# Kernel tuning notes

Measured on AMD Instinct MI355X. Metric: run time of the kernel, lower is better.

The kernel has to match this reference:

```python
import jax, jax.numpy as jnp
import numpy as np

HIDDEN = 2048
N_HEADS = 16
N_KV_HEADS = 8
HEAD_DIM = 128
ROTARY_DIM = 32  # int(128 * 0.25), already even
ROPE_THETA = 10000000.0
EPS = 1e-6
BATCH, SEQ = 2, 2048


def _rmsnorm(x, w, eps=EPS):
    # per-head RMSNorm over last dim; weight is zero-init, scale = 1 + w
    r = jax.lax.rsqrt(jnp.mean(x * x, axis=-1, keepdims=True) + eps)
    return x * r * (1.0 + w)


def _rope(x, positions, rotary_dim, theta):
    # x: [b, s, h, rotary_dim]; rotate-halves RoPE
    half = rotary_dim // 2
    inv_freq = 1.0 / (theta ** (jnp.arange(half, dtype=jnp.float32) / half))
    ang = positions.astype(jnp.float32)[:, :, None] * inv_freq  # [b, s, half]
    cos = jnp.cos(ang)[:, :, None, :]
    sin = jnp.sin(ang)[:, :, None, :]
    x1, x2 = x[..., :half], x[..., half:]
    return jnp.concatenate([x1 * cos - x2 * sin, x1 * sin + x2 * cos], axis=-1)


def setup_inputs() -> dict:
    key = jax.random.key(0)
    ks = jax.random.split(key, 8)
    scale = lambda fan_in: 1.0 / np.sqrt(fan_in)
    x = jax.random.normal(ks[0], (BATCH, SEQ, HIDDEN), dtype=jnp.float32)
    Wq = jax.random.normal(ks[1], (HIDDEN, N_HEADS * HEAD_DIM * 2), jnp.float32) * scale(HIDDEN)
    Wk = jax.random.normal(ks[2], (HIDDEN, N_KV_HEADS * HEAD_DIM), jnp.float32) * scale(HIDDEN)
    Wv = jax.random.normal(ks[3], (HIDDEN, N_KV_HEADS * HEAD_DIM), jnp.float32) * scale(HIDDEN)
    Wo = jax.random.normal(ks[4], (N_HEADS * HEAD_DIM, HIDDEN), jnp.float32) * scale(N_HEADS * HEAD_DIM)
    q_norm_w = jax.random.normal(ks[5], (HEAD_DIM,), jnp.float32) * 0.02
    k_norm_w = jax.random.normal(ks[6], (HEAD_DIM,), jnp.float32) * 0.02
    attention_mask = jnp.ones((BATCH, SEQ), dtype=jnp.int32)
    positions = jnp.broadcast_to(jnp.arange(SEQ, dtype=jnp.int32), (BATCH, SEQ))
    return {"x": x, "attention_mask": attention_mask, "positions": positions,
            "Wq": Wq, "Wk": Wk, "Wv": Wv, "Wo": Wo,
            "q_norm_w": q_norm_w, "k_norm_w": k_norm_w}


def reference(x, attention_mask, positions, Wq, Wk, Wv, Wo, q_norm_w, k_norm_w):
    b, s, _ = x.shape
    g = N_HEADS // N_KV_HEADS  # GQA group size

    q_all = jnp.einsum('bsh,ho->bso', x, Wq).reshape(b, s, N_HEADS, HEAD_DIM * 2)
    q, gate = jnp.split(q_all, 2, axis=-1)          # each [b,s,H,D]
    gate = gate.reshape(b, s, N_HEADS * HEAD_DIM)
    q = _rmsnorm(q, q_norm_w)
    k = _rmsnorm(jnp.einsum('bsh,ho->bso', x, Wk).reshape(b, s, N_KV_HEADS, HEAD_DIM), k_norm_w)
    v = jnp.einsum('bsh,ho->bso', x, Wv).reshape(b, s, N_KV_HEADS, HEAD_DIM)

    # partial RoPE on first ROTARY_DIM dims
    q = jnp.concatenate([_rope(q[..., :ROTARY_DIM], positions, ROTARY_DIM, ROPE_THETA), q[..., ROTARY_DIM:]], axis=-1)
    k = jnp.concatenate([_rope(k[..., :ROTARY_DIM], positions, ROTARY_DIM, ROPE_THETA), k[..., ROTARY_DIM:]], axis=-1)

    # grouped-query causal attention
    qg = q.reshape(b, s, N_KV_HEADS, g, HEAD_DIM)
    scores = jnp.einsum('bqhgd,bkhd->bhgqk', qg, k) / jnp.sqrt(jnp.float32(HEAD_DIM))
    causal = jnp.tril(jnp.ones((s, s), dtype=bool))
    key_valid = attention_mask.astype(bool)[:, None, None, None, :]  # [b,1,1,1,k]
    mask = causal[None, None, None, :, :] & key_valid
    scores = jnp.where(mask, scores, jnp.finfo(scores.dtype).min)
    probs = jax.nn.softmax(scores, axis=-1)
    attn = jnp.einsum('bhgqk,bkhd->bqhgd', probs, v).reshape(b, s, N_HEADS * HEAD_DIM)

    attn = attn * jax.nn.sigmoid(gate)
    return jnp.einsum('bso,oh->bsh', attn, Wo)
```

## Files before the change

### kernel.cpp

```cpp
#include <hip/hip_runtime.h>
#include <cstdint>

typedef __bf16  bf16;
typedef __bf16  bf16x8 __attribute__((ext_vector_type(8)));
typedef __bf16  bf16x4 __attribute__((ext_vector_type(4)));
typedef __bf16  bf16x2 __attribute__((ext_vector_type(2)));
typedef float   f32x4  __attribute__((ext_vector_type(4)));
typedef float   f32x16 __attribute__((ext_vector_type(16)));

#define GLOAD_LDS16(g, l) __builtin_amdgcn_global_load_lds( \
    (const __attribute__((address_space(1))) void*)(g),     \
    (__attribute__((address_space(3))) void*)(l), 16, 0, 0)

#define SEQ   2048
#define HID   2048
#define NH    16
#define NKV   8
#define HD    128
#define NQKV  6144
#define MTOT  4096

__device__ __forceinline__ void transw_body(const float* __restrict__ W, bf16* __restrict__ WT,
                                            int N, int n0, int k0, int t) {
    __shared__ float tile[64][65];
    int tn = t & 63, t4 = t >> 6;
    #pragma unroll
    for (int i = 0; i < 16; ++i) {
        int kk = i * 4 + t4;
        tile[kk][tn] = W[(size_t)(k0 + kk) * N + n0 + tn];
    }
    __syncthreads();
    int tk8 = (t & 7) * 8;
    int tnn = t >> 3;
    #pragma unroll
    for (int i = 0; i < 2; ++i) {
        int nn = i * 32 + tnn;
        bf16x8 o;
        #pragma unroll
        for (int j = 0; j < 8; ++j) o[j] = (bf16)tile[tk8 + j][nn];
        *(bf16x8*)(&WT[(size_t)(n0 + nn) * HID + k0 + tk8]) = o;
    }
}

__global__ __launch_bounds__(256) void prep_kernel(const float* __restrict__ x, bf16* __restrict__ xb,
                                                   const float* __restrict__ Wq, const float* __restrict__ Wk,
                                                   const float* __restrict__ Wv, const float* __restrict__ Wo,
                                                   bf16* __restrict__ wqkvT, bf16* __restrict__ woT) {
    int bx = blockIdx.x, t = threadIdx.x;
    if (bx < 4096) {
        int i = bx * 256 + t;
        f32x4 v0 = ((const f32x4*)x)[i * 2];
        f32x4 v1 = ((const f32x4*)x)[i * 2 + 1];
        bf16x8 o;
        o[0] = (bf16)v0[0]; o[1] = (bf16)v0[1]; o[2] = (bf16)v0[2]; o[3] = (bf16)v0[3];
        o[4] = (bf16)v1[0]; o[5] = (bf16)v1[1]; o[6] = (bf16)v1[2]; o[7] = (bf16)v1[3];
        ((bf16x8*)xb)[i] = o;
    } else if (bx < 4096 + 2048) {
        int idx = bx - 4096;
        transw_body(Wq, wqkvT, 4096, (idx & 63) * 64, (idx >> 6) * 64, t);
    } else if (bx < 4096 + 2048 + 512) {
        int idx = bx - (4096 + 2048);
        transw_body(Wk, wqkvT + (size_t)4096 * HID, 1024, (idx & 15) * 64, (idx >> 4) * 64, t);
    } else if (bx < 4096 + 2048 + 1024) {
        int idx = bx - (4096 + 2048 + 512);
        transw_body(Wv, wqkvT + (size_t)5120 * HID, 1024, (idx & 15) * 64, (idx >> 4) * 64, t);
    } else {
        int idx = bx - (4096 + 2048 + 1024);
        transw_body(Wo, woT, 2048, (idx & 31) * 64, (idx >> 5) * 64, t);
    }
}

template<bool OUT_BF16>
__global__ __launch_bounds__(256) void gemm_bt(const bf16* __restrict__ A, const bf16* __restrict__ Bt,
                                               void* __restrict__ C, int M, int N, int K) {
    __shared__ __align__(16) bf16 As[128 * 64];
    __shared__ __align__(16) bf16 Bs[128 * 64];
    const int tid = threadIdx.x;
    const int wave = tid >> 6, lane = tid & 63;
    const int l31 = lane & 31, half = lane >> 5;
    const int tile_n = blockIdx.x * 128, tile_m = blockIdx.y * 128;
    const int wm = (wave & 1) * 64, wn = (wave >> 1) * 64;
    const int sw = l31 & 7;
    f32x16 acc[2][2] = {};

    for (int k0 = 0; k0 < K; k0 += 64) {
        __syncthreads();
        #pragma unroll
        for (int j = 0; j < 4; ++j) {
            int s = j * 256 + tid;
            int row = s >> 3, c = s & 7;
            int cs = c ^ (row & 7);
            GLOAD_LDS16(A  + (size_t)(tile_m + row) * K + k0 + (cs << 3), As + (size_t)s * 8);
            GLOAD_LDS16(Bt + (size_t)(tile_n + row) * K + k0 + (cs << 3), Bs + (size_t)s * 8);
        }
        __syncthreads();
        #pragma unroll
        for (int ks = 0; ks < 4; ++ks) {
            int ch = ((ks * 2 + half) ^ sw) << 3;
            bf16x8 a0 = *(const bf16x8*)(As + (size_t)(wm + l31) * 64 + ch);
            bf16x8 a1 = *(const bf16x8*)(As + (size_t)(wm + 32 + l31) * 64 + ch);
            bf16x8 b0 = *(const bf16x8*)(Bs + (size_t)(wn + l31) * 64 + ch);
            bf16x8 b1 = *(const bf16x8*)(Bs + (size_t)(wn + 32 + l31) * 64 + ch);
            acc[0][0] = __builtin_amdgcn_mfma_f32_32x32x16_bf16(a0, b0, acc[0][0], 0, 0, 0);
            acc[0][1] = __builtin_amdgcn_mfma_f32_32x32x16_bf16(a0, b1, acc[0][1], 0, 0, 0);
            acc[1][0] = __builtin_amdgcn_mfma_f32_32x32x16_bf16(a1, b0, acc[1][0], 0, 0, 0);
            acc[1][1] = __builtin_amdgcn_mfma_f32_32x32x16_bf16(a1, b1, acc[1][1], 0, 0, 0);
        }
    }
    #pragma unroll
    for (int mt = 0; mt < 2; ++mt)
        #pragma unroll
        for (int nt = 0; nt < 2; ++nt)
            #pragma unroll
            for (int reg = 0; reg < 16; ++reg) {
                int row = tile_m + wm + mt * 32 + (reg & 3) + ((reg >> 2) * 8) + half * 4;
                int col = tile_n + wn + nt * 32 + l31;
                float v = acc[mt][nt][reg];
                if (OUT_BF16) ((bf16*)C)[(size_t)row * N + col] = (bf16)v;
                else          ((float*)C)[(size_t)row * N + col] = v;
            }
}

__global__ __launch_bounds__(256) void post_kernel(const bf16* __restrict__ qkv,
                                                   const float* __restrict__ qnw, const float* __restrict__ knw,
                                                   const int* __restrict__ positions,
                                                   bf16* __restrict__ Qh, bf16* __restrict__ Kh,
                                                   bf16* __restrict__ VT) {
    int bx = blockIdx.x;
    if (bx < 4096) {
        int tk = bx;
        int b = tk >> 11, s = tk & 2047;
        int wave = threadIdx.x >> 6, lane = threadIdx.x & 63;
        int g16 = lane >> 4;
        int l16 = lane & 15;
        int d0 = l16 * 8;
        float pos = (float)positions[tk];
        const float L = 1.4533435415278355f;

        float cv[8], sv[8];
        if (l16 < 4) {
            #pragma unroll
            for (int j = 0; j < 8; ++j) {
                float a = pos * exp2f(-(float)((l16 & 1) * 8 + j) * L);
                cv[j] = cosf(a); sv[j] = sinf(a);
            }
        }

        #pragma unroll
        for (int i = 0; i < 2; ++i) {
            int slot = i * 16 + wave * 4 + g16;
            if (slot >= 24) continue;
            bool isq = (slot < 16);
            int h = isq ? slot : slot - 16;
            const bf16* base = qkv + (size_t)tk * NQKV + (isq ? h * 256 : 4096 + h * HD) + d0;
            bf16x8 v = *(const bf16x8*)base;
            float f[8];
            float ssq = 0.0f;
            #pragma unroll
            for (int j = 0; j < 8; ++j) { f[j] = (float)v[j]; ssq += f[j] * f[j]; }
            #pragma unroll
            for (int off = 8; off; off >>= 1) ssq += __shfl_xor(ssq, off);
            float rn = rsqrtf(ssq * (1.0f / 128.0f) + 1e-6f);
            const float* nw = isq ? qnw : knw;
            f32x4 wa = *(const f32x4*)(nw + d0);
            f32x4 wb = *(const f32x4*)(nw + d0 + 4);
            float xv[8];
            #pragma unroll
            for (int j = 0; j < 4; ++j) { xv[j] = f[j] * rn * (1.0f + wa[j]); xv[j + 4] = f[j + 4] * rn * (1.0f + wb[j]); }
            float out[8];
            #pragma unroll
            for (int j = 0; j < 8; ++j) out[j] = xv[j];
            if (l16 < 4) {
                #pragma unroll
                for (int j = 0; j < 8; ++j) {
                    float p = __shfl_xor(xv[j], 2);
                    out[j] = (l16 < 2) ? (xv[j] * cv[j] - p * sv[j])
                                       : (xv[j] * cv[j] + p * sv[j]);
                }
            }
            bf16x8 o;
            #pragma unroll
            for (int j = 0; j < 8; ++j) o[j] = (bf16)out[j];
            bf16* dst = isq ? (Qh + ((size_t)(b * NH + h) * SEQ + s) * HD)
                            : (Kh + ((size_t)(b * NKV + h) * SEQ + s) * HD);
            *(bf16x8*)(dst + d0) = o;
        }
    } else {
        int idx = bx - 4096;
        int bh = idx >> 5, st = idx & 31;
        int b = bh >> 3, h = bh & 7;
        __shared__ float tile[64][129];
        int t = threadIdx.x;
        const bf16* src = qkv + ((size_t)(b * SEQ) + st * 64) * NQKV + 5120 + h * HD;
        #pragma unroll
        for (int i = 0; i < 32; ++i) {
            int ii = i * 256 + t;
            int tok = ii >> 7, d = ii & 127;
            tile[tok][d] = (float)src[(size_t)tok * NQKV + d];
        }
        __syncthreads();
        bf16* dst = VT + (size_t)(b * NKV + h) * HD * SEQ + st * 64;
        #pragma unroll
        for (int i = 0; i < 32; ++i) {
            int ii = i * 256 + t;
            int d = ii >> 6, sx = ii & 63;
            dst[(size_t)d * SEQ + sx] = (bf16)tile[sx][d];
        }
    }
}

__global__ __launch_bounds__(512, 4) void attn_kernel(const bf16* __restrict__ Qh, const bf16* __restrict__ Kh,
                                                      const bf16* __restrict__ VT, const bf16* __restrict__ qkv,
                                                      const int* __restrict__ amask, bf16* __restrict__ attnb) {
    const int bx = blockIdx.x;
    const int hb = (bx >> 4) & 31;
    const int head = hb & 15, b = hb >> 4;
    int q0 = ((bx & 15) + hb) & 15;
    const int qt = (bx & 256) ? (15 - q0) : q0;
    const int kvh = head >> 1;
    __shared__ __align__(16) bf16 Ks[2][64 * 128];
    __shared__ __align__(16) bf16 Vs[2][128 * 64];
    __shared__ __align__(16) bf16 Ps[8 * 16 * 64];
    const int tid = threadIdx.x, wave = tid >> 6, lane = tid & 63;
    const int quad = lane >> 4, cl = lane & 15;

    const bf16* qsrc = Qh + ((size_t)(b * NH + head) * SEQ + qt * 128) * HD;
    bf16x8 aq[4];
    #pragma unroll
    for (int kc = 0; kc < 4; ++kc)
        aq[kc] = *(const bf16x8*)(qsrc + (size_t)(wave * 16 + cl) * HD + kc * 32 + quad * 8);

    float lstate[4] = {0.0f, 0.0f, 0.0f, 0.0f};
    f32x4 oacc[8] = {};
    const int qrow_glob = qt * 128 + wave * 16 + quad * 4;
    const float scale = 0.08838834764831845f * 1.4426950408889634f;
    const float M = 20.0f;
    const int kmax = 2 * qt + 1;

    const bf16* kbase = Kh + (size_t)(b * NKV + kvh) * SEQ * HD;
    const bf16* vbase = VT + (size_t)(b * NKV + kvh) * HD * SEQ;

#define STAGE_KV(kt_, buf_) { \
    const bf16* ksrc = kbase + (size_t)(kt_) * 64 * HD; \
    const bf16* vsrc = vbase + (size_t)(kt_) * 64; \
    _Pragma("unroll") \
    for (int j = 0; j < 2; ++j) { \
        int s = j * 512 + tid;                     \
        int rK = s >> 4, cK = s & 15; \
        GLOAD_LDS16(ksrc + (size_t)rK * HD + ((cK ^ (rK & 15)) << 3), &Ks[buf_][0] + (size_t)s * 8); \
        int dV = s >> 3, cV = s & 7; \
        GLOAD_LDS16(vsrc + (size_t)dV * SEQ + ((cV ^ (dV & 7)) << 3), &Vs[buf_][0] + (size_t)s * 8); \
    } }

    STAGE_KV(0, 0);
    int cur = 0;
    for (int kt = 0; kt <= kmax; ++kt) {
        __syncthreads();
        int mv = amask[b * SEQ + kt * 64 + lane];
        if (kt < kmax) STAGE_KV(kt + 1, cur ^ 1);

        f32x4 sc[4] = {};
        #pragma unroll
        for (int nt = 0; nt < 4; ++nt)
            #pragma unroll
            for (int kc = 0; kc < 4; ++kc) {
                bf16x8 bk = *(const bf16x8*)(&Ks[cur][0] + (size_t)(nt * 16 + cl) * 128 + (((kc * 4 + quad) ^ cl) << 3));
                sc[nt] = __builtin_amdgcn_mfma_f32_16x16x32_bf16(aq[kc], bk, sc[nt], 0, 0, 0);
            }

        unsigned long long mbits = __ballot(mv != 0);
        #pragma unroll
        for (int nt = 0; nt < 4; ++nt) {
            int kcol = kt * 64 + nt * 16 + cl;
            bool cok = (mbits >> (nt * 16 + cl)) & 1ull;
            #pragma unroll
            for (int r = 0; r < 4; ++r) {
                bool ok = cok && (kcol <= qrow_glob + r);
                float p = ok ? exp2f(sc[nt][r] * scale - M) : 0.0f;
                lstate[r] += p;
                Ps[wave * 1024 + (quad * 4 + r) * 64 + ((nt * 16 + cl) ^ (quad << 4))] = (bf16)p;
            }
        }

        bf16x8 ap[2];
        #pragma unroll
        for (int c = 0; c < 2; ++c)
            ap[c] = *(const bf16x8*)(Ps + wave * 1024 + cl * 64 + ((c * 32 + quad * 8) ^ ((cl >> 2) << 4)));
        #pragma unroll
        for (int n2 = 0; n2 < 8; ++n2)
            #pragma unroll
            for (int c = 0; c < 2; ++c) {
                bf16x8 bv = *(const bf16x8*)(&Vs[cur][0] + (size_t)(n2 * 16 + cl) * 64 + (((c * 4 + quad) ^ (cl & 7)) << 3));
                oacc[n2] = __builtin_amdgcn_mfma_f32_16x16x32_bf16(ap[c], bv, oacc[n2], 0, 0, 0);
            }
        cur ^= 1;
    }
#undef STAGE_KV

    #pragma unroll
    for (int r = 0; r < 4; ++r) {
        #pragma unroll
        for (int off = 8; off; off >>= 1) lstate[r] += __shfl_xor(lstate[r], off);
        int srow = qt * 128 + wave * 16 + quad * 4 + r;
        float linv = 1.0f / lstate[r];
        #pragma unroll
        for (int n2 = 0; n2 < 8; ++n2) {
            int d = n2 * 16 + cl;
            float g = (float)qkv[(size_t)(b * SEQ + srow) * NQKV + head * 256 + 128 + d];
            float sig = 1.0f / (1.0f + __expf(-g));
            float v = oacc[n2][r] * linv * sig;
            attnb[(size_t)(b * SEQ + srow) * HID + head * HD + d] = (bf16)v;
        }
    }
}

extern "C" void kernel_launch(void* const* d_in, const int* in_sizes, int n_in,
                              void* d_out, int out_size, void* d_ws, size_t ws_size,
                              hipStream_t stream) {
    const float* x        = (const float*)d_in[0];
    const int*   amask    = (const int*)d_in[1];
    const int*   positions= (const int*)d_in[2];
    const float* Wq       = (const float*)d_in[3];
    const float* Wk       = (const float*)d_in[4];
    const float* Wv       = (const float*)d_in[5];
    const float* Wo       = (const float*)d_in[6];
    const float* qnw      = (const float*)d_in[7];
    const float* knw      = (const float*)d_in[8];
    float* out = (float*)d_out;
    char* ws = (char*)d_ws;

    bf16* xb    = (bf16*)(ws);
    bf16* wqkvT = (bf16*)(ws + 16777216);
    bf16* woT   = (bf16*)(ws + 41943040);
    bf16* qkv   = (bf16*)(ws + 50331648);
    bf16* Qh    = (bf16*)(ws + 100663296);
    bf16* Kh    = (bf16*)(ws + 117440512);
    bf16* VT    = (bf16*)(ws + 125829120);
    bf16* attnb = (bf16*)(ws + 134217728);

    prep_kernel<<<8192, 256, 0, stream>>>(x, xb, Wq, Wk, Wv, Wo, wqkvT, woT);
    gemm_bt<true><<<dim3(48, 32), 256, 0, stream>>>(xb, wqkvT, qkv, MTOT, NQKV, HID);
    post_kernel<<<4608, 256, 0, stream>>>(qkv, qnw, knw, positions, Qh, Kh, VT);
    attn_kernel<<<512, 512, 0, stream>>>(Qh, Kh, VT, qkv, amask, attnb);
    gemm_bt<false><<<dim3(16, 32), 256, 0, stream>>>(attnb, woT, out, MTOT, HID, HID);

    (void)in_sizes; (void)n_in; (void)out_size; (void)ws_size;
}
```

Measured before the change: 399.8 us.

## Process two 16-row query groups per wave with 4-wave attention blocks

The attention block is cut from 8 waves to 4, and each wave now handles 32 query rows (two 16-row groups). Each K and V fragment read from LDS is reused for two MFMAs, which halves LDS traffic per unit of matrix work. Scheduling priority is raised around the MFMA sections with s_setprio. In exchange, each wave holds twice the accumulators and Q registers, and there are fewer waves per block to hide latency.

```diff
diff --git a/kernel.cpp b/kernel.cpp
--- a/kernel.cpp
+++ b/kernel.cpp
@@ -209,7 +209,7 @@
     }
 }
 
-__global__ __launch_bounds__(512, 4) void attn_kernel(const bf16* __restrict__ Qh, const bf16* __restrict__ Kh,
+__global__ __launch_bounds__(256, 2) void attn_kernel(const bf16* __restrict__ Qh, const bf16* __restrict__ Kh,
                                                       const bf16* __restrict__ VT, const bf16* __restrict__ qkv,
                                                       const int* __restrict__ amask, bf16* __restrict__ attnb) {
     const int bx = blockIdx.x;
@@ -220,19 +220,21 @@
     const int kvh = head >> 1;
     __shared__ __align__(16) bf16 Ks[2][64 * 128];
     __shared__ __align__(16) bf16 Vs[2][128 * 64];
-    __shared__ __align__(16) bf16 Ps[8 * 16 * 64];
+    __shared__ __align__(16) bf16 Ps[4 * 32 * 64];
     const int tid = threadIdx.x, wave = tid >> 6, lane = tid & 63;
     const int quad = lane >> 4, cl = lane & 15;
 
     const bf16* qsrc = Qh + ((size_t)(b * NH + head) * SEQ + qt * 128) * HD;
-    bf16x8 aq[4];
-    #pragma unroll
-    for (int kc = 0; kc < 4; ++kc)
-        aq[kc] = *(const bf16x8*)(qsrc + (size_t)(wave * 16 + cl) * HD + kc * 32 + quad * 8);
-
-    float lstate[4] = {0.0f, 0.0f, 0.0f, 0.0f};
-    f32x4 oacc[8] = {};
-    const int qrow_glob = qt * 128 + wave * 16 + quad * 4;
+    bf16x8 aq[2][4];
+    #pragma unroll
+    for (int rg = 0; rg < 2; ++rg)
+        #pragma unroll
+        for (int kc = 0; kc < 4; ++kc)
+            aq[rg][kc] = *(const bf16x8*)(qsrc + (size_t)(wave * 32 + rg * 16 + cl) * HD + kc * 32 + quad * 8);
+
+    float lstate[2][4] = {};
+    f32x4 oacc[2][8] = {};
+    const int qrow_glob0 = qt * 128 + wave * 32 + quad * 4;
     const float scale = 0.08838834764831845f * 1.4426950408889634f;
     const float M = 20.0f;
     const int kmax = 2 * qt + 1;
@@ -244,8 +246,8 @@
     const bf16* ksrc = kbase + (size_t)(kt_) * 64 * HD; \
     const bf16* vsrc = vbase + (size_t)(kt_) * 64; \
     _Pragma("unroll") \
-    for (int j = 0; j < 2; ++j) { \
-        int s = j * 512 + tid;                     \
+    for (int j = 0; j < 4; ++j) { \
+        int s = j * 256 + tid;                     \
         int rK = s >> 4, cK = s & 15; \
         GLOAD_LDS16(ksrc + (size_t)rK * HD + ((cK ^ (rK & 15)) << 3), &Ks[buf_][0] + (size_t)s * 8); \
         int dV = s >> 3, cV = s & 7; \
@@ -259,59 +261,71 @@
         int mv = amask[b * SEQ + kt * 64 + lane];
         if (kt < kmax) STAGE_KV(kt + 1, cur ^ 1);
 
-        f32x4 sc[4] = {};
+        f32x4 sc[2][4] = {};
+        __builtin_amdgcn_s_setprio(1);
         #pragma unroll
         for (int nt = 0; nt < 4; ++nt)
             #pragma unroll
             for (int kc = 0; kc < 4; ++kc) {
                 bf16x8 bk = *(const bf16x8*)(&Ks[cur][0] + (size_t)(nt * 16 + cl) * 128 + (((kc * 4 + quad) ^ cl) << 3));
-                sc[nt] = __builtin_amdgcn_mfma_f32_16x16x32_bf16(aq[kc], bk, sc[nt], 0, 0, 0);
-            }
+                sc[0][nt] = __builtin_amdgcn_mfma_f32_16x16x32_bf16(aq[0][kc], bk, sc[0][nt], 0, 0, 0);
+                sc[1][nt] = __builtin_amdgcn_mfma_f32_16x16x32_bf16(aq[1][kc], bk, sc[1][nt], 0, 0, 0);
+            }
+        __builtin_amdgcn_s_setprio(0);
 
         unsigned long long mbits = __ballot(mv != 0);
         #pragma unroll
-        for (int nt = 0; nt < 4; ++nt) {
-            int kcol = kt * 64 + nt * 16 + cl;
-            bool cok = (mbits >> (nt * 16 + cl)) & 1ull;
-            #pragma unroll
-            for (int r = 0; r < 4; ++r) {
-                bool ok = cok && (kcol <= qrow_glob + r);
-                float p = ok ? exp2f(sc[nt][r] * scale - M) : 0.0f;
-                lstate[r] += p;
-                Ps[wave * 1024 + (quad * 4 + r) * 64 + ((nt * 16 + cl) ^ (quad << 4))] = (bf16)p;
-            }
-        }
-
-        bf16x8 ap[2];
-        #pragma unroll
-        for (int c = 0; c < 2; ++c)
-            ap[c] = *(const bf16x8*)(Ps + wave * 1024 + cl * 64 + ((c * 32 + quad * 8) ^ ((cl >> 2) << 4)));
+        for (int rg = 0; rg < 2; ++rg)
+            #pragma unroll
+            for (int nt = 0; nt < 4; ++nt) {
+                int kcol = kt * 64 + nt * 16 + cl;
+                bool cok = (mbits >> (nt * 16 + cl)) & 1ull;
+                #pragma unroll
+                for (int r = 0; r < 4; ++r) {
+                    bool ok = cok && (kcol <= qrow_glob0 + rg * 16 + r);
+                    float p = ok ? exp2f(sc[rg][nt][r] * scale - M) : 0.0f;
+                    lstate[rg][r] += p;
+                    Ps[wave * 2048 + (rg * 16 + quad * 4 + r) * 64 + ((nt * 16 + cl) ^ (quad << 4))] = (bf16)p;
+                }
+            }
+
+        bf16x8 ap[2][2];
+        #pragma unroll
+        for (int rg = 0; rg < 2; ++rg)
+            #pragma unroll
+            for (int c = 0; c < 2; ++c)
+                ap[rg][c] = *(const bf16x8*)(Ps + wave * 2048 + (rg * 16 + cl) * 64 + ((c * 32 + quad * 8) ^ ((cl >> 2) << 4)));
+        __builtin_amdgcn_s_setprio(1);
         #pragma unroll
         for (int n2 = 0; n2 < 8; ++n2)
             #pragma unroll
             for (int c = 0; c < 2; ++c) {
                 bf16x8 bv = *(const bf16x8*)(&Vs[cur][0] + (size_t)(n2 * 16 + cl) * 64 + (((c * 4 + quad) ^ (cl & 7)) << 3));
-                oacc[n2] = __builtin_amdgcn_mfma_f32_16x16x32_bf16(ap[c], bv, oacc[n2], 0, 0, 0);
-            }
+                oacc[0][n2] = __builtin_amdgcn_mfma_f32_16x16x32_bf16(ap[0][c], bv, oacc[0][n2], 0, 0, 0);
+                oacc[1][n2] = __builtin_amdgcn_mfma_f32_16x16x32_bf16(ap[1][c], bv, oacc[1][n2], 0, 0, 0);
+            }
+        __builtin_amdgcn_s_setprio(0);
         cur ^= 1;
     }
 #undef STAGE_KV
 
     #pragma unroll
-    for (int r = 0; r < 4; ++r) {
-        #pragma unroll
-        for (int off = 8; off; off >>= 1) lstate[r] += __shfl_xor(lstate[r], off);
-        int srow = qt * 128 + wave * 16 + quad * 4 + r;
-        float linv = 1.0f / lstate[r];
-        #pragma unroll
-        for (int n2 = 0; n2 < 8; ++n2) {
-            int d = n2 * 16 + cl;
-            float g = (float)qkv[(size_t)(b * SEQ + srow) * NQKV + head * 256 + 128 + d];
-            float sig = 1.0f / (1.0f + __expf(-g));
-            float v = oacc[n2][r] * linv * sig;
-            attnb[(size_t)(b * SEQ + srow) * HID + head * HD + d] = (bf16)v;
-        }
-    }
+    for (int rg = 0; rg < 2; ++rg)
+        #pragma unroll
+        for (int r = 0; r < 4; ++r) {
+            #pragma unroll
+            for (int off = 8; off; off >>= 1) lstate[rg][r] += __shfl_xor(lstate[rg][r], off);
+            int srow = qt * 128 + wave * 32 + rg * 16 + quad * 4 + r;
+            float linv = 1.0f / lstate[rg][r];
+            #pragma unroll
+            for (int n2 = 0; n2 < 8; ++n2) {
+                int d = n2 * 16 + cl;
+                float g = (float)qkv[(size_t)(b * SEQ + srow) * NQKV + head * 256 + 128 + d];
+                float sig = 1.0f / (1.0f + __expf(-g));
+                float v = oacc[rg][n2][r] * linv * sig;
+                attnb[(size_t)(b * SEQ + srow) * HID + head * HD + d] = (bf16)v;
+            }
+        }
 }
 
 extern "C" void kernel_launch(void* const* d_in, const int* in_sizes, int n_in,
@@ -341,7 +355,7 @@
     prep_kernel<<<8192, 256, 0, stream>>>(x, xb, Wq, Wk, Wv, Wo, wqkvT, woT);
     gemm_bt<true><<<dim3(48, 32), 256, 0, stream>>>(xb, wqkvT, qkv, MTOT, NQKV, HID);
     post_kernel<<<4608, 256, 0, stream>>>(qkv, qnw, knw, positions, Qh, Kh, VT);
-    attn_kernel<<<512, 512, 0, stream>>>(Qh, Kh, VT, qkv, amask, attnb);
+    attn_kernel<<<512, 256, 0, stream>>>(Qh, Kh, VT, qkv, amask, attnb);
     gemm_bt<false><<<dim3(16, 32), 256, 0, stream>>>(attnb, woT, out, MTOT, HID, HID);
 
     (void)in_sizes; (void)n_in; (void)out_size; (void)ws_size;
```

Result: slower. 409.6 us (+2.5%).
